# Kernel optimization log

Hardware: AMD Instinct MI355X
Metric: run time of the kernel (lower is better)

## Reference

```python
import jax, jax.numpy as jnp
import numpy as np

B, N, DIM_IN, DIM_OUT, EMBED, DP = 8, 1024, 64, 64, 16, 16


def setup_inputs() -> dict:
    key = jax.random.key(0)
    k1, k2, k3, k4, k5 = jax.random.split(key, 5)
    x = jax.random.normal(k1, (B, N, DIM_IN), dtype=jnp.float32)
    node_embed = jax.random.normal(k2, (N, EMBED), dtype=jnp.float32)
    prompt_answer = jax.random.normal(k3, (B, N, DP), dtype=jnp.float32)
    # kaiming-normal-like init for the pools (gain irrelevant for correctness testing)
    weights_pool = jax.random.normal(k4, (EMBED, 2, DIM_IN, DIM_OUT), dtype=jnp.float32) * (2.0 / (2 * DIM_IN * DIM_OUT)) ** 0.5
    bias_pool = jax.random.normal(k5, (EMBED, DIM_OUT), dtype=jnp.float32) * (2.0 / DIM_OUT) ** 0.5
    return {"x": x, "node_embed": node_embed, "prompt_answer": prompt_answer,
            "weights_pool": weights_pool, "bias_pool": bias_pool}


def reference(x, node_embed, prompt_answer, weights_pool, bias_pool):
    n = node_embed.shape[0]
    # adaptive adjacency: softmax(relu(E E^T)) over rows' last dim (torch dim=1 on 2D)
    sim = jax.nn.softmax(jax.nn.relu(node_embed @ node_embed.T), axis=1)  # [N,N]
    supports = jnp.stack([jnp.eye(n, dtype=x.dtype), sim], axis=0)        # [2,N,N]
    # node-adaptive weights/bias
    weights = jnp.einsum('nd,dkio->nkio', node_embed, weights_pool)       # [N,2,I,O]
    bias = node_embed @ bias_pool                                         # [N,O]
    # sub-support from L1 cdist; torch softmax dim=1 of [B,N,N] -> axis=1
    d1 = jnp.sum(jnp.abs(prompt_answer[:, :, None, :] - prompt_answer[:, None, :, :]), axis=-1)  # [B,N,N]
    sub = jax.nn.softmax(-jax.nn.relu(d1), axis=1)                        # [B,N,N]
    # supports' = supports @ sub (sub expanded over k=2); then x_g = supports' @ x.
    # Associate as supports @ (sub @ x) to avoid the [B,2,N,N] intermediate.
    sx = jnp.einsum('bmc,bcd->bmd', sub, x)                               # [B,N,I]  (sub @ x)
    x_g = jnp.einsum('knm,bmc->bknc', supports, sx)                       # [B,2,N,I]
    x_g = jnp.transpose(x_g, (0, 2, 1, 3))                                # [B,N,2,I]
    return jnp.einsum('bnki,nkio->bno', x_g, weights) + bias              # [B,N,O]
```

## Files before the change

### kernel.cpp

```cpp
#include <hip/hip_runtime.h>

#define BB 8
#define NN 1024
#define DIN 64
#define DOUT 64
#define EMB 16
#define DPC 16

typedef __attribute__((ext_vector_type(8))) short bf16x8;
typedef __attribute__((ext_vector_type(4))) float f32x4;

__device__ inline unsigned short f2bf(float f) {
    unsigned u = __float_as_uint(f);
    u += 0x7fffu + ((u >> 16) & 1u);
    return (unsigned short)(u >> 16);
}

__global__ __launch_bounds__(256) void k_front(const float* __restrict__ E,
                                               const float* __restrict__ pa,
                                               const float* __restrict__ x,
                                               const float* __restrict__ wp,
                                               unsigned short* __restrict__ sim_bf,
                                               unsigned short* __restrict__ Sub,
                                               unsigned short* __restrict__ xzT,
                                               unsigned short* __restrict__ WPT) {
    __shared__ __align__(16) char smem[36096];
    const int bid = blockIdx.x;
    const int tid = threadIdx.x;

    if (bid < 256) {
        const int b = bid >> 5, c0 = (bid & 31) * 32;
        float* pa_l  = (float*)smem;
        float* myp   = (float*)(smem + 32768);
        float* zpart = (float*)(smem + 34816);
        float* invZ  = (float*)(smem + 35840);

        if (tid < 128)
            ((float4*)myp)[tid] = *(const float4*)&pa[((size_t)b*NN + c0)*DPC + tid*4];
        __syncthreads();

        const int cs = tid & 31, jq = tid >> 5;
        float myc[DPC];
        #pragma unroll
        for (int p4 = 0; p4 < 4; ++p4) {
            float4 t = *(const float4*)&myp[cs*DPC + p4*4];
            myc[p4*4+0] = t.x; myc[p4*4+1] = t.y; myc[p4*4+2] = t.z; myc[p4*4+3] = t.w;
        }

        float part = 0.0f;
        for (int h = 0; h < 2; ++h) {
            __syncthreads();
            for (int i = tid; i < 512*DPC/4; i += 256)
                ((float4*)pa_l)[i] = ((const float4*)(pa + ((size_t)b*NN + h*512)*DPC))[i];
            __syncthreads();
            unsigned short* subrow = Sub + ((size_t)b*NN + (c0 + cs))*NN + h*512 + jq*64;
            for (int j4 = 0; j4 < 16; ++j4) {
                float e[4];
                #pragma unroll
                for (int t = 0; t < 4; ++t) {
                    int jj = jq*64 + j4*4 + t;
                    float s = 0.0f;
                    #pragma unroll
                    for (int p4 = 0; p4 < 4; ++p4) {
                        float4 q = *(const float4*)&pa_l[jj*DPC + p4*4];
                        s += fabsf(myc[p4*4+0]-q.x) + fabsf(myc[p4*4+1]-q.y)
                           + fabsf(myc[p4*4+2]-q.z) + fabsf(myc[p4*4+3]-q.w);
                    }
                    e[t] = __expf(-s);
                }
                part += e[0] + e[1] + e[2] + e[3];
                *(ushort4*)&subrow[j4*4] =
                    make_ushort4(f2bf(e[0]), f2bf(e[1]), f2bf(e[2]), f2bf(e[3]));
            }
        }
        zpart[jq*32 + cs] = part;
        __syncthreads();
        float* xl = pa_l;
        #pragma unroll
        for (int i = 0; i < 8; ++i) {
            int l = i*256 + tid, d = l & 63, c = l >> 6;
            xl[c*65 + d] = x[((size_t)b*NN + c0 + c)*DIN + d];
        }
        if (tid < 32) {
            float z = 0.f;
            #pragma unroll
            for (int q = 0; q < 8; ++q) z += zpart[q*32 + tid];
            invZ[tid] = 1.0f / z;
        }
        __syncthreads();
        #pragma unroll
        for (int i = 0; i < 8; ++i) {
            int l = i*256 + tid, c = l & 31, d = l >> 5;
            xzT[((size_t)b*DIN + d)*NN + c0 + c] = f2bf(xl[c*65 + d] * invZ[c]);
        }
    } else if (bid < 1280) {
        const int i = bid - 256;
        const int lane = tid & 63, wave = tid >> 6;
        float* redw = (float*)smem;

        float4 ei0 = *(const float4*)&E[i*EMB + 0];
        float4 ei1 = *(const float4*)&E[i*EMB + 4];
        float4 ei2 = *(const float4*)&E[i*EMB + 8];
        float4 ei3 = *(const float4*)&E[i*EMB + 12];

        float rv[4], tmax = -1e30f;
        #pragma unroll
        for (int k = 0; k < 4; ++k) {
            int j = tid + k*256;
            float4 a0 = *(const float4*)&E[j*EMB + 0];
            float4 a1 = *(const float4*)&E[j*EMB + 4];
            float4 a2 = *(const float4*)&E[j*EMB + 8];
            float4 a3 = *(const float4*)&E[j*EMB + 12];
            float s = ei0.x*a0.x + ei0.y*a0.y + ei0.z*a0.z + ei0.w*a0.w
                    + ei1.x*a1.x + ei1.y*a1.y + ei1.z*a1.z + ei1.w*a1.w
                    + ei2.x*a2.x + ei2.y*a2.y + ei2.z*a2.z + ei2.w*a2.w
                    + ei3.x*a3.x + ei3.y*a3.y + ei3.z*a3.z + ei3.w*a3.w;
            s = fmaxf(s, 0.0f);
            rv[k] = s; tmax = fmaxf(tmax, s);
        }
        #pragma unroll
        for (int off = 32; off > 0; off >>= 1) tmax = fmaxf(tmax, __shfl_xor(tmax, off));
        if (lane == 0) redw[wave] = tmax;
        __syncthreads();
        float rmax = fmaxf(fmaxf(redw[0], redw[1]), fmaxf(redw[2], redw[3]));
        __syncthreads();

        float ev[4], tsum = 0.f;
        #pragma unroll
        for (int k = 0; k < 4; ++k) { ev[k] = __expf(rv[k] - rmax); tsum += ev[k]; }
        #pragma unroll
        for (int off = 32; off > 0; off >>= 1) tsum += __shfl_xor(tsum, off);
        if (lane == 0) redw[wave] = tsum;
        __syncthreads();
        float inv = 1.0f / (redw[0] + redw[1] + redw[2] + redw[3]);
        #pragma unroll
        for (int k = 0; k < 4; ++k)
            sim_bf[(size_t)i*NN + tid + k*256] = f2bf(ev[k] * inv);
    } else {
        const int d = bid - 1280;
        float* wpl = (float*)smem;
        const float* wsrc = wp + (size_t)d * 8192;
        for (int i = tid; i < 2048; i += 256)
            ((float4*)wpl)[i] = ((const float4*)wsrc)[i];
        __syncthreads();
        const int o = tid & 63, g = tid >> 6;
        #pragma unroll
        for (int k = 0; k < 2; ++k) {
            unsigned short tmp[16];
            #pragma unroll
            for (int t = 0; t < 16; ++t)
                tmp[t] = f2bf(wpl[k*4096 + (g*16 + t)*64 + o]);
            unsigned short* dst = WPT + (size_t)(d*64 + o)*128 + k*64 + g*16;
            #pragma unroll
            for (int t4 = 0; t4 < 4; ++t4)
                *(ushort4*)&dst[t4*4] =
                    make_ushort4(tmp[t4*4], tmp[t4*4+1], tmp[t4*4+2], tmp[t4*4+3]);
        }
    }
}

#define ASTR 72
#define BSTR 72

__device__ inline void gemm_tile32(const unsigned short* __restrict__ Arow,
                                   const unsigned short* __restrict__ Brow,
                                   unsigned short* A_l, unsigned short* B_l,
                                   int tid, f32x4& acc0, f32x4& acc1) {
    const int lane = tid & 63, wave = tid >> 6;
    const int q = lane >> 4, r = lane & 15;

    const int brow_ = tid >> 2, bch = (tid & 3) * 2;
    const int arow_ = tid >> 3, ach = tid & 7;

    uint4 pb0 = *(const uint4*)&Brow[(size_t)brow_*NN + (bch+0)*8];
    uint4 pb1 = *(const uint4*)&Brow[(size_t)brow_*NN + (bch+1)*8];
    uint4 pa0 = *(const uint4*)&Arow[(size_t)arow_*NN + ach*8];

    for (int kk = 0; kk < 16; ++kk) {
        __syncthreads();
        *(uint4*)&B_l[brow_*BSTR + (bch+0)*8] = pb0;
        *(uint4*)&B_l[brow_*BSTR + (bch+1)*8] = pb1;
        *(uint4*)&A_l[arow_*ASTR + ach*8] = pa0;
        __syncthreads();
        if (kk < 15) {
            int c1 = (kk + 1) * 64;
            pb0 = *(const uint4*)&Brow[(size_t)brow_*NN + c1 + (bch+0)*8];
            pb1 = *(const uint4*)&Brow[(size_t)brow_*NN + c1 + (bch+1)*8];
            pa0 = *(const uint4*)&Arow[(size_t)arow_*NN + c1 + ach*8];
        }
        #pragma unroll
        for (int ks = 0; ks < 2; ++ks) {
            bf16x8 bfr = *(const bf16x8*)&B_l[(wave*16 + r)*BSTR + ks*32 + q*8];
            bf16x8 a0 = *(const bf16x8*)&A_l[r*ASTR + ks*32 + q*8];
            acc0 = __builtin_amdgcn_mfma_f32_16x16x32_bf16(a0, bfr, acc0, 0, 0, 0);
            bf16x8 a1 = *(const bf16x8*)&A_l[(16 + r)*ASTR + ks*32 + q*8];
            acc1 = __builtin_amdgcn_mfma_f32_16x16x32_bf16(a1, bfr, acc1, 0, 0, 0);
        }
    }
}

__global__ __launch_bounds__(256) void k_sx4(const unsigned short* __restrict__ Sub,
                                             const unsigned short* __restrict__ xzT,
                                             unsigned short* __restrict__ sx_bf,
                                             unsigned short* __restrict__ sxT) {
    const int b = blockIdx.y, m0 = blockIdx.x * 32;
    const int tid = threadIdx.x, lane = tid & 63, wave = tid >> 6;
    __shared__ __align__(16) unsigned short A_l[32 * ASTR];
    __shared__ __align__(16) unsigned short B_l[64 * BSTR];

    f32x4 acc0 = {0.f, 0.f, 0.f, 0.f}, acc1 = {0.f, 0.f, 0.f, 0.f};
    gemm_tile32(Sub + ((size_t)b*NN + m0)*NN, xzT + (size_t)b*DIN*NN, A_l, B_l, tid, acc0, acc1);

    const int q = lane >> 4, r = lane & 15;
    const int d = wave*16 + r;
    #pragma unroll
    for (int rt = 0; rt < 2; ++rt) {
        const f32x4& acc = rt ? acc1 : acc0;
        const int mrow = m0 + rt*16 + q*4;
        unsigned short h0 = f2bf(acc[0]), h1 = f2bf(acc[1]), h2 = f2bf(acc[2]), h3 = f2bf(acc[3]);
        sx_bf[((size_t)b*NN + mrow + 0)*DIN + d] = h0;
        sx_bf[((size_t)b*NN + mrow + 1)*DIN + d] = h1;
        sx_bf[((size_t)b*NN + mrow + 2)*DIN + d] = h2;
        sx_bf[((size_t)b*NN + mrow + 3)*DIN + d] = h3;
        *(ushort4*)&sxT[((size_t)b*DIN + d)*NN + mrow] = make_ushort4(h0, h1, h2, h3);
    }
}

#define S2 136
#define PSTR 65

__global__ __launch_bounds__(256) void k_y_out(const unsigned short* __restrict__ sim_bf,
                                               const unsigned short* __restrict__ sxT,
                                               const unsigned short* __restrict__ sx_bf,
                                               const unsigned short* __restrict__ WPT,
                                               const float* __restrict__ E,
                                               const float* __restrict__ bp,
                                               float* __restrict__ out) {
    const int b = blockIdx.y, m0 = blockIdx.x * 32;
    const int tid = threadIdx.x, lane = tid & 63, wave = tid >> 6;
    __shared__ __align__(16) unsigned short A_l[32 * ASTR];
    __shared__ __align__(16) unsigned short B_l[64 * BSTR];
    __shared__ __align__(16) unsigned short A2[32 * S2];
    __shared__ float E32[32 * EMB];
    __shared__ float bpl[EMB * DOUT];
    __shared__ float part[4 * 32 * PSTR];

    if (tid < 128)
        ((float4*)E32)[tid] = ((const float4*)&E[(size_t)m0 * EMB])[tid];
    ((float4*)bpl)[tid] = ((const float4*)bp)[tid];
    {
        int row = tid >> 3, c8 = (tid & 7) * 8;
        *(uint4*)&A2[row*S2 + c8] =
            *(const uint4*)&sx_bf[((size_t)b*NN + m0 + row)*DIN + c8];
    }

    f32x4 acc0 = {0.f, 0.f, 0.f, 0.f}, acc1 = {0.f, 0.f, 0.f, 0.f};
    gemm_tile32(sim_bf + (size_t)m0*NN, sxT + (size_t)b*DIN*NN, A_l, B_l, tid, acc0, acc1);

    const int q = lane >> 4, r = lane & 15;
    #pragma unroll
    for (int reg = 0; reg < 4; ++reg)
        A2[(q*4 + reg)*S2 + 64 + wave*16 + r] = f2bf(acc0[reg]);
    #pragma unroll
    for (int reg = 0; reg < 4; ++reg)
        A2[(16 + q*4 + reg)*S2 + 64 + wave*16 + r] = f2bf(acc1[reg]);
    __syncthreads();

    bf16x8 af[2][4];
    #pragma unroll
    for (int rt = 0; rt < 2; ++rt)
        #pragma unroll
        for (int ks = 0; ks < 4; ++ks)
            af[rt][ks] = *(const bf16x8*)&A2[(rt*16 + r)*S2 + ks*32 + q*8];

    f32x4 pacc[2][16];
    #pragma unroll
    for (int rt = 0; rt < 2; ++rt)
        #pragma unroll
        for (int i = 0; i < 16; ++i) pacc[rt][i] = (f32x4){0.f, 0.f, 0.f, 0.f};

    const unsigned short* wbase = WPT + ((size_t)(wave*256 + r))*128 + q*8;
    #pragma unroll
    for (int nfl = 0; nfl < 16; ++nfl) {
        const unsigned short* bb = wbase + (size_t)nfl * 16 * 128;
        #pragma unroll
        for (int ks = 0; ks < 4; ++ks) {
            bf16x8 bf_ = *(const bf16x8*)(bb + ks*32);
            pacc[0][nfl] = __builtin_amdgcn_mfma_f32_16x16x32_bf16(af[0][ks], bf_, pacc[0][nfl], 0, 0, 0);
            pacc[1][nfl] = __builtin_amdgcn_mfma_f32_16x16x32_bf16(af[1][ks], bf_, pacc[1][nfl], 0, 0, 0);
        }
    }

    float po[2][4][4];
    #pragma unroll
    for (int rt = 0; rt < 2; ++rt)
        #pragma unroll
        for (int reg = 0; reg < 4; ++reg)
            #pragma unroll
            for (int ohi = 0; ohi < 4; ++ohi) po[rt][reg][ohi] = 0.f;
    #pragma unroll
    for (int nfl = 0; nfl < 16; ++nfl) {
        const int dd = nfl >> 2, ohi = nfl & 3;
        #pragma unroll
        for (int rt = 0; rt < 2; ++rt)
            #pragma unroll
            for (int reg = 0; reg < 4; ++reg)
                po[rt][reg][ohi] += E32[(rt*16 + q*4 + reg)*EMB + wave*4 + dd] * pacc[rt][nfl][reg];
    }
    #pragma unroll
    for (int rt = 0; rt < 2; ++rt)
        #pragma unroll
        for (int reg = 0; reg < 4; ++reg)
            #pragma unroll
            for (int ohi = 0; ohi < 4; ++ohi)
                part[wave*32*PSTR + (rt*16 + q*4 + reg)*PSTR + ohi*16 + r] = po[rt][reg][ohi];
    __syncthreads();

    #pragma unroll
    for (int g = 0; g < 2; ++g) {
        const int idx = g*256 + tid;
        const int row = idx >> 4, o4 = (idx & 15) * 4;
        float4 res;
        #pragma unroll
        for (int j = 0; j < 4; ++j) {
            const int o = o4 + j;
            float s = part[0*32*PSTR + row*PSTR + o] + part[1*32*PSTR + row*PSTR + o]
                    + part[2*32*PSTR + row*PSTR + o] + part[3*32*PSTR + row*PSTR + o];
            float bsum = 0.f;
            #pragma unroll
            for (int d = 0; d < EMB; ++d)
                bsum += E32[row*EMB + d] * bpl[d*DOUT + o];
            ((float*)&res)[j] = s + bsum;
        }
        *(float4*)&out[((size_t)b*NN + m0 + row)*DOUT + o4] = res;
    }
}

extern "C" void kernel_launch(void* const* d_in, const int* in_sizes, int n_in,
                              void* d_out, int out_size, void* d_ws, size_t ws_size,
                              hipStream_t stream) {
    (void)in_sizes; (void)n_in; (void)out_size; (void)ws_size;
    const float* x  = (const float*)d_in[0];
    const float* E  = (const float*)d_in[1];
    const float* pa = (const float*)d_in[2];
    const float* wp = (const float*)d_in[3];
    const float* bp = (const float*)d_in[4];
    float* out = (float*)d_out;

    unsigned short* ws16   = (unsigned short*)d_ws;
    unsigned short* sim_bf = ws16;
    unsigned short* xzT    = sim_bf + (size_t)NN*NN;
    unsigned short* sxT    = xzT + (size_t)BB*DIN*NN;
    unsigned short* Sub    = sxT + (size_t)BB*DIN*NN;
    unsigned short* sx_bf  = Sub + (size_t)BB*NN*NN;
    unsigned short* WPT    = sx_bf + (size_t)BB*NN*DIN;

    k_front<<<1296, 256, 0, stream>>>(E, pa, x, wp, sim_bf, Sub, xzT, WPT);
    k_sx4<<<dim3(32, BB), 256, 0, stream>>>(Sub, xzT, sx_bf, sxT);
    k_y_out<<<dim3(32, BB), 256, 0, stream>>>(sim_bf, sxT, sx_bf, WPT, E, bp, out);
}
```

Measured before the change: 115.1 us.

## Fuse sub-support, sx GEMM and output into one persistent kernel with grid barriers

Moves the L1-distance softmax numerator computation into a persistent 256-block kernel that keeps each block's 32x1024 Sub tile in LDS instead of writing the full B*N*N bf16 Sub matrix to global memory. The sx GEMM then reads Sub straight from LDS, and two software grid barriers separate the phases that need xzT and sxT from every block. The sim and weight-pool preparation moves into a separate preceding kernel, which also resets the barrier counters. This removes a large global write and read of Sub and a kernel launch, at the cost of relying on all 256 blocks being co-resident and on spin-wait barriers, using about 100KB of LDS per block.

Measured after the change: 203.3 us. 1.77x slower.

```diff
diff --git a/kernel.cpp b/kernel.cpp
--- a/kernel.cpp
+++ b/kernel.cpp
@@ -16,87 +16,21 @@
     return (unsigned short)(u >> 16);
 }
 
-__global__ __launch_bounds__(256) void k_front(const float* __restrict__ E,
-                                               const float* __restrict__ pa,
-                                               const float* __restrict__ x,
-                                               const float* __restrict__ wp,
-                                               unsigned short* __restrict__ sim_bf,
-                                               unsigned short* __restrict__ Sub,
-                                               unsigned short* __restrict__ xzT,
-                                               unsigned short* __restrict__ WPT) {
-    __shared__ __align__(16) char smem[36096];
+__global__ __launch_bounds__(256) void k_sp(const float* __restrict__ E,
+                                            const float* __restrict__ wp,
+                                            unsigned short* __restrict__ sim_bf,
+                                            unsigned short* __restrict__ WPT,
+                                            unsigned* __restrict__ bar) {
+    __shared__ __align__(16) char smem[32768];
+    __shared__ float redw[4];
     const int bid = blockIdx.x;
     const int tid = threadIdx.x;
 
-    if (bid < 256) {
-        const int b = bid >> 5, c0 = (bid & 31) * 32;
-        float* pa_l  = (float*)smem;
-        float* myp   = (float*)(smem + 32768);
-        float* zpart = (float*)(smem + 34816);
-        float* invZ  = (float*)(smem + 35840);
-
-        if (tid < 128)
-            ((float4*)myp)[tid] = *(const float4*)&pa[((size_t)b*NN + c0)*DPC + tid*4];
-        __syncthreads();
-
-        const int cs = tid & 31, jq = tid >> 5;
-        float myc[DPC];
-        #pragma unroll
-        for (int p4 = 0; p4 < 4; ++p4) {
-            float4 t = *(const float4*)&myp[cs*DPC + p4*4];
-            myc[p4*4+0] = t.x; myc[p4*4+1] = t.y; myc[p4*4+2] = t.z; myc[p4*4+3] = t.w;
-        }
-
-        float part = 0.0f;
-        for (int h = 0; h < 2; ++h) {
-            __syncthreads();
-            for (int i = tid; i < 512*DPC/4; i += 256)
-                ((float4*)pa_l)[i] = ((const float4*)(pa + ((size_t)b*NN + h*512)*DPC))[i];
-            __syncthreads();
-            unsigned short* subrow = Sub + ((size_t)b*NN + (c0 + cs))*NN + h*512 + jq*64;
-            for (int j4 = 0; j4 < 16; ++j4) {
-                float e[4];
-                #pragma unroll
-                for (int t = 0; t < 4; ++t) {
-                    int jj = jq*64 + j4*4 + t;
-                    float s = 0.0f;
-                    #pragma unroll
-                    for (int p4 = 0; p4 < 4; ++p4) {
-                        float4 q = *(const float4*)&pa_l[jj*DPC + p4*4];
-                        s += fabsf(myc[p4*4+0]-q.x) + fabsf(myc[p4*4+1]-q.y)
-                           + fabsf(myc[p4*4+2]-q.z) + fabsf(myc[p4*4+3]-q.w);
-                    }
-                    e[t] = __expf(-s);
-                }
-                part += e[0] + e[1] + e[2] + e[3];
-                *(ushort4*)&subrow[j4*4] =
-                    make_ushort4(f2bf(e[0]), f2bf(e[1]), f2bf(e[2]), f2bf(e[3]));
-            }
-        }
-        zpart[jq*32 + cs] = part;
-        __syncthreads();
-        float* xl = pa_l;
-        #pragma unroll
-        for (int i = 0; i < 8; ++i) {
-            int l = i*256 + tid, d = l & 63, c = l >> 6;
-            xl[c*65 + d] = x[((size_t)b*NN + c0 + c)*DIN + d];
-        }
-        if (tid < 32) {
-            float z = 0.f;
-            #pragma unroll
-            for (int q = 0; q < 8; ++q) z += zpart[q*32 + tid];
-            invZ[tid] = 1.0f / z;
-        }
-        __syncthreads();
-        #pragma unroll
-        for (int i = 0; i < 8; ++i) {
-            int l = i*256 + tid, c = l & 31, d = l >> 5;
-            xzT[((size_t)b*DIN + d)*NN + c0 + c] = f2bf(xl[c*65 + d] * invZ[c]);
-        }
-    } else if (bid < 1280) {
-        const int i = bid - 256;
+    if (bid == 0 && tid == 0) { bar[0] = 0u; bar[1] = 0u; }
+
+    if (bid < 1024) {
+        const int i = bid;
         const int lane = tid & 63, wave = tid >> 6;
-        float* redw = (float*)smem;
 
         float4 ei0 = *(const float4*)&E[i*EMB + 0];
         float4 ei1 = *(const float4*)&E[i*EMB + 4];
@@ -137,7 +71,7 @@
         for (int k = 0; k < 4; ++k)
             sim_bf[(size_t)i*NN + tid + k*256] = f2bf(ev[k] * inv);
     } else {
-        const int d = bid - 1280;
+        const int d = bid - 1024;
         float* wpl = (float*)smem;
         const float* wsrc = wp + (size_t)d * 8192;
         for (int i = tid; i < 2048; i += 256)
@@ -157,6 +91,18 @@
                     make_ushort4(tmp[t4*4], tmp[t4*4+1], tmp[t4*4+2], tmp[t4*4+3]);
         }
     }
+}
+
+__device__ inline void grid_barrier(unsigned* cnt) {
+    __threadfence();
+    __syncthreads();
+    if (threadIdx.x == 0) {
+        atomicAdd(cnt, 1u);
+        while (__hip_atomic_load(cnt, __ATOMIC_RELAXED, __HIP_MEMORY_SCOPE_AGENT) < 256u)
+            __builtin_amdgcn_s_sleep(1);
+    }
+    __syncthreads();
+    __threadfence();
 }
 
 #define ASTR 72
@@ -199,71 +145,154 @@
     }
 }
 
-__global__ __launch_bounds__(256) void k_sx4(const unsigned short* __restrict__ Sub,
-                                             const unsigned short* __restrict__ xzT,
-                                             unsigned short* __restrict__ sx_bf,
-                                             unsigned short* __restrict__ sxT) {
-    const int b = blockIdx.y, m0 = blockIdx.x * 32;
-    const int tid = threadIdx.x, lane = tid & 63, wave = tid >> 6;
-    __shared__ __align__(16) unsigned short A_l[32 * ASTR];
-    __shared__ __align__(16) unsigned short B_l[64 * BSTR];
-
-    f32x4 acc0 = {0.f, 0.f, 0.f, 0.f}, acc1 = {0.f, 0.f, 0.f, 0.f};
-    gemm_tile32(Sub + ((size_t)b*NN + m0)*NN, xzT + (size_t)b*DIN*NN, A_l, B_l, tid, acc0, acc1);
-
-    const int q = lane >> 4, r = lane & 15;
-    const int d = wave*16 + r;
-    #pragma unroll
-    for (int rt = 0; rt < 2; ++rt) {
-        const f32x4& acc = rt ? acc1 : acc0;
-        const int mrow = m0 + rt*16 + q*4;
-        unsigned short h0 = f2bf(acc[0]), h1 = f2bf(acc[1]), h2 = f2bf(acc[2]), h3 = f2bf(acc[3]);
-        sx_bf[((size_t)b*NN + mrow + 0)*DIN + d] = h0;
-        sx_bf[((size_t)b*NN + mrow + 1)*DIN + d] = h1;
-        sx_bf[((size_t)b*NN + mrow + 2)*DIN + d] = h2;
-        sx_bf[((size_t)b*NN + mrow + 3)*DIN + d] = h3;
-        *(ushort4*)&sxT[((size_t)b*DIN + d)*NN + mrow] = make_ushort4(h0, h1, h2, h3);
-    }
-}
-
+#define SUB_STR 1032
 #define S2 136
 #define PSTR 65
-
-__global__ __launch_bounds__(256) void k_y_out(const unsigned short* __restrict__ sim_bf,
-                                               const unsigned short* __restrict__ sxT,
-                                               const unsigned short* __restrict__ sx_bf,
-                                               const unsigned short* __restrict__ WPT,
-                                               const float* __restrict__ E,
-                                               const float* __restrict__ bp,
-                                               float* __restrict__ out) {
-    const int b = blockIdx.y, m0 = blockIdx.x * 32;
-    const int tid = threadIdx.x, lane = tid & 63, wave = tid >> 6;
-    __shared__ __align__(16) unsigned short A_l[32 * ASTR];
-    __shared__ __align__(16) unsigned short B_l[64 * BSTR];
-    __shared__ __align__(16) unsigned short A2[32 * S2];
-    __shared__ float E32[32 * EMB];
-    __shared__ float bpl[EMB * DOUT];
-    __shared__ float part[4 * 32 * PSTR];
+#define SM_BYTES 102016
+
+__global__ __launch_bounds__(256) void k_main(const float* __restrict__ E,
+                                              const float* __restrict__ pa,
+                                              const float* __restrict__ x,
+                                              const unsigned short* __restrict__ sim_bf,
+                                              unsigned short* __restrict__ xzT,
+                                              unsigned short* __restrict__ sxT,
+                                              const unsigned short* __restrict__ WPT,
+                                              const float* __restrict__ bp,
+                                              float* __restrict__ out,
+                                              unsigned* __restrict__ bar) {
+    __shared__ __align__(16) char smem[SM_BYTES];
+    unsigned short* Sub_l = (unsigned short*)smem;
+    const int bid = blockIdx.x, tid = threadIdx.x;
+    const int b = bid >> 5, m0 = (bid & 31) * 32;
+    const int lane = tid & 63, wave = tid >> 6;
+    const int q = lane >> 4, r = lane & 15;
+
+    {
+        float* pa_l  = (float*)(smem + 66048);
+        float* myp   = (float*)(smem + 98816);
+        float* zpart = (float*)(smem + 100864);
+        float* invZ  = (float*)(smem + 101888);
+
+        if (tid < 128)
+            ((float4*)myp)[tid] = *(const float4*)&pa[((size_t)b*NN + m0)*DPC + tid*4];
+        __syncthreads();
+
+        const int cs = tid & 31, jq = tid >> 5;
+        float myc[DPC];
+        #pragma unroll
+        for (int p4 = 0; p4 < 4; ++p4) {
+            float4 t = *(const float4*)&myp[cs*DPC + p4*4];
+            myc[p4*4+0] = t.x; myc[p4*4+1] = t.y; myc[p4*4+2] = t.z; myc[p4*4+3] = t.w;
+        }
+
+        float partv = 0.0f;
+        for (int h = 0; h < 2; ++h) {
+            __syncthreads();
+            for (int i = tid; i < 512*DPC/4; i += 256)
+                ((float4*)pa_l)[i] = ((const float4*)(pa + ((size_t)b*NN + h*512)*DPC))[i];
+            __syncthreads();
+            unsigned short* subrow = Sub_l + cs*SUB_STR + h*512 + jq*64;
+            for (int j4 = 0; j4 < 16; ++j4) {
+                float e[4];
+                #pragma unroll
+                for (int t = 0; t < 4; ++t) {
+                    int jj = jq*64 + j4*4 + t;
+                    float s = 0.0f;
+                    #pragma unroll
+                    for (int p4 = 0; p4 < 4; ++p4) {
+                        float4 qv = *(const float4*)&pa_l[jj*DPC + p4*4];
+                        s += fabsf(myc[p4*4+0]-qv.x) + fabsf(myc[p4*4+1]-qv.y)
+                           + fabsf(myc[p4*4+2]-qv.z) + fabsf(myc[p4*4+3]-qv.w);
+                    }
+                    e[t] = __expf(-s);
+                }
+                partv += e[0] + e[1] + e[2] + e[3];
+                *(ushort4*)&subrow[j4*4] =
+                    make_ushort4(f2bf(e[0]), f2bf(e[1]), f2bf(e[2]), f2bf(e[3]));
+            }
+        }
+        zpart[jq*32 + cs] = partv;
+        __syncthreads();
+        float* xl = pa_l;
+        #pragma unroll
+        for (int i = 0; i < 8; ++i) {
+            int l = i*256 + tid, d = l & 63, c = l >> 6;
+            xl[c*65 + d] = x[((size_t)b*NN + m0 + c)*DIN + d];
+        }
+        if (tid < 32) {
+            float z = 0.f;
+            #pragma unroll
+            for (int qi = 0; qi < 8; ++qi) z += zpart[qi*32 + tid];
+            invZ[tid] = 1.0f / z;
+        }
+        __syncthreads();
+        #pragma unroll
+        for (int i = 0; i < 8; ++i) {
+            int l = i*256 + tid, c = l & 31, d = l >> 5;
+            xzT[((size_t)b*DIN + d)*NN + m0 + c] = f2bf(xl[c*65 + d] * invZ[c]);
+        }
+    }
+    grid_barrier(&bar[0]);
+
+    f32x4 acc0 = {0.f, 0.f, 0.f, 0.f}, acc1 = {0.f, 0.f, 0.f, 0.f};
+    {
+        const unsigned short* Bb = xzT + ((size_t)b*DIN + wave*16 + r)*NN;
+        const int q8 = q * 8;
+        #pragma unroll
+        for (int kk = 0; kk < 16; ++kk) {
+            #pragma unroll
+            for (int ks = 0; ks < 2; ++ks) {
+                const int cb = kk*64 + ks*32 + q8;
+                bf16x8 bfr = *(const bf16x8*)&Bb[cb];
+                bf16x8 a0 = *(const bf16x8*)&Sub_l[r*SUB_STR + cb];
+                acc0 = __builtin_amdgcn_mfma_f32_16x16x32_bf16(a0, bfr, acc0, 0, 0, 0);
+                bf16x8 a1 = *(const bf16x8*)&Sub_l[(16 + r)*SUB_STR + cb];
+                acc1 = __builtin_amdgcn_mfma_f32_16x16x32_bf16(a1, bfr, acc1, 0, 0, 0);
+            }
+        }
+    }
+    __syncthreads();
+    unsigned short* A2 = (unsigned short*)(smem + 44032);
+    {
+        const int d = wave*16 + r;
+        {
+            const int mrow = m0 + q*4;
+            unsigned short h0 = f2bf(acc0[0]), h1 = f2bf(acc0[1]),
+                           h2 = f2bf(acc0[2]), h3 = f2bf(acc0[3]);
+            *(ushort4*)&sxT[((size_t)b*DIN + d)*NN + mrow] = make_ushort4(h0, h1, h2, h3);
+            A2[(q*4 + 0)*S2 + d] = h0;  A2[(q*4 + 1)*S2 + d] = h1;
+            A2[(q*4 + 2)*S2 + d] = h2;  A2[(q*4 + 3)*S2 + d] = h3;
+        }
+        {
+            const int mrow = m0 + 16 + q*4;
+            unsigned short h0 = f2bf(acc1[0]), h1 = f2bf(acc1[1]),
+                           h2 = f2bf(acc1[2]), h3 = f2bf(acc1[3]);
+            *(ushort4*)&sxT[((size_t)b*DIN + d)*NN + mrow] = make_ushort4(h0, h1, h2, h3);
+            A2[(16 + q*4 + 0)*S2 + d] = h0;  A2[(16 + q*4 + 1)*S2 + d] = h1;
+            A2[(16 + q*4 + 2)*S2 + d] = h2;  A2[(16 + q*4 + 3)*S2 + d] = h3;
+        }
+    }
+    grid_barrier(&bar[1]);
+
+    unsigned short* A_l = (unsigned short*)smem;
+    float* part = (float*)(smem + 4608);
+    float* E32  = (float*)(smem + 37888);
+    float* bpl  = (float*)(smem + 39936);
+    unsigned short* B_l = (unsigned short*)(smem + 66048);
 
     if (tid < 128)
         ((float4*)E32)[tid] = ((const float4*)&E[(size_t)m0 * EMB])[tid];
     ((float4*)bpl)[tid] = ((const float4*)bp)[tid];
-    {
-        int row = tid >> 3, c8 = (tid & 7) * 8;
-        *(uint4*)&A2[row*S2 + c8] =
-            *(const uint4*)&sx_bf[((size_t)b*NN + m0 + row)*DIN + c8];
-    }
-
-    f32x4 acc0 = {0.f, 0.f, 0.f, 0.f}, acc1 = {0.f, 0.f, 0.f, 0.f};
-    gemm_tile32(sim_bf + (size_t)m0*NN, sxT + (size_t)b*DIN*NN, A_l, B_l, tid, acc0, acc1);
-
-    const int q = lane >> 4, r = lane & 15;
+
+    f32x4 y0 = {0.f, 0.f, 0.f, 0.f}, y1 = {0.f, 0.f, 0.f, 0.f};
+    gemm_tile32(sim_bf + (size_t)m0*NN, sxT + (size_t)b*DIN*NN, A_l, B_l, tid, y0, y1);
+
     #pragma unroll
     for (int reg = 0; reg < 4; ++reg)
-        A2[(q*4 + reg)*S2 + 64 + wave*16 + r] = f2bf(acc0[reg]);
+        A2[(q*4 + reg)*S2 + 64 + wave*16 + r] = f2bf(y0[reg]);
     #pragma unroll
     for (int reg = 0; reg < 4; ++reg)
-        A2[(16 + q*4 + reg)*S2 + 64 + wave*16 + r] = f2bf(acc1[reg]);
+        A2[(16 + q*4 + reg)*S2 + 64 + wave*16 + r] = f2bf(y1[reg]);
     __syncthreads();
 
     bf16x8 af[2][4];
@@ -351,11 +380,9 @@
     unsigned short* sim_bf = ws16;
     unsigned short* xzT    = sim_bf + (size_t)NN*NN;
     unsigned short* sxT    = xzT + (size_t)BB*DIN*NN;
-    unsigned short* Sub    = sxT + (size_t)BB*DIN*NN;
-    unsigned short* sx_bf  = Sub + (size_t)BB*NN*NN;
-    unsigned short* WPT    = sx_bf + (size_t)BB*NN*DIN;
-
-    k_front<<<1296, 256, 0, stream>>>(E, pa, x, wp, sim_bf, Sub, xzT, WPT);
-    k_sx4<<<dim3(32, BB), 256, 0, stream>>>(Sub, xzT, sx_bf, sxT);
-    k_y_out<<<dim3(32, BB), 256, 0, stream>>>(sim_bf, sxT, sx_bf, WPT, E, bp, out);
-}
+    unsigned short* WPT    = sxT + (size_t)BB*DIN*NN;
+    unsigned* bar          = (unsigned*)(WPT + (size_t)131072);
+
+    k_sp<<<1040, 256, 0, stream>>>(E, wp, sim_bf, WPT, bar);
+    k_main<<<256, 256, 0, stream>>>(E, pa, x, sim_bf, xzT, sxT, WPT, bp, out, bar);
+}
```
